# Kernel tuning notes

Hardware: AMD Instinct MI355X
Metric: run time of the kernel (lower is better)

Reference implementation:

```python
import jax, jax.numpy as jnp
import numpy as np

K_NEIGHBORS = 8  # hard-coded k in extract_edge_features
NUM_HEADS = 12


def _sqdist(a, b):
    # a [B,M,3], b [B,N,3] -> squared euclidean distances [B,M,N]
    # (monotone in cdist, so argmax/top-k indices are identical to torch.cdist)
    return jnp.sum((a[:, :, None, :] - b[:, None, :, :]) ** 2, axis=-1)


def _fps(points, num_samples):
    # Farthest point sampling (intended semantics of farthest_point_sampling):
    # iteratively pick the point maximizing the min distance to the selected set.
    B, N, _ = points.shape
    bidx = jnp.arange(B)

    def d_to(idx):  # idx [B] -> squared dist from points[b, idx[b]] to all points [B,N]
        p = points[bidx, idx]  # [B,3]
        return jnp.sum((points - p[:, None, :]) ** 2, axis=-1)

    idx0 = jnp.zeros((B,), jnp.int32)  # deterministic start point

    def step(min_d, _):
        nxt = jnp.argmax(min_d, axis=-1).astype(jnp.int32)  # [B]
        min_d = jnp.minimum(min_d, d_to(nxt))
        return min_d, nxt

    _, rest = jax.lax.scan(step, d_to(idx0), None, length=num_samples - 1)  # rest [M-1,B]
    idxs = jnp.concatenate([idx0[None, :], rest], axis=0).T  # [B,M]
    return jnp.take_along_axis(points, idxs[:, :, None], axis=1)  # [B,M,3]


def _edge_features(points, features, k=K_NEIGHBORS):
    # EdgeAligner.extract_edge_features: kNN by cdist+topk(smallest), then
    # edge = feature - mean(neighbor features)
    d2 = _sqdist(points, points)  # [B,M,M]
    _, nn_idx = jax.lax.top_k(-d2, k)  # [B,M,k] indices of k nearest (incl. self)
    nbr = jax.vmap(lambda f, idx: f[idx])(features, nn_idx)  # [B,M,k,D]
    return features - jnp.mean(nbr, axis=2)


def _mha(x, Wq, bq, Wk, bk, Wv, bv, Wo, bo, num_heads=NUM_HEADS):
    # standard torch nn.MultiheadAttention (self-attention, batch_first)
    B, S, D = x.shape
    dh = D // num_heads
    split = lambda t: t.reshape(B, S, num_heads, dh).transpose(0, 2, 1, 3)
    q = split(x @ Wq + bq)
    k = split(x @ Wk + bk)
    v = split(x @ Wv + bv)
    scale = jnp.asarray(1.0 / np.sqrt(dh), x.dtype)
    att = jax.nn.softmax(jnp.einsum('bhqd,bhkd->bhqk', q, k) * scale, axis=-1)
    o = jnp.einsum('bhqk,bhkd->bhqd', att, v)  # [B,H,S,dh]
    o = o.transpose(0, 2, 1, 3).reshape(B, S, D)
    return o @ Wo + bo


def setup_inputs() -> dict:
    key = jax.random.key(0)
    ks = jax.random.split(key, 8)
    B, N, D = 4, 8192, 768
    s = 0.02
    return {
        'points': jax.random.normal(ks[0], (B, N, 3), jnp.float32),
        'W_embed': jax.random.normal(ks[1], (3, D), jnp.float32) * s,
        'b_embed': jnp.zeros((D,), jnp.float32),
        'Wq': jax.random.normal(ks[2], (D, D), jnp.float32) * s,
        'bq': jnp.zeros((D,), jnp.float32),
        'Wk': jax.random.normal(ks[3], (D, D), jnp.float32) * s,
        'bk': jnp.zeros((D,), jnp.float32),
        'Wv': jax.random.normal(ks[4], (D, D), jnp.float32) * s,
        'bv': jnp.zeros((D,), jnp.float32),
        'Wo': jax.random.normal(ks[5], (D, D), jnp.float32) * s,
        'bo': jnp.zeros((D,), jnp.float32),
        'Ws': jax.random.normal(ks[6], (3, D), jnp.float32) * s,
        'bs': jnp.zeros((D,), jnp.float32),
        'num_samples': 1024,
    }


def reference(points, W_embed, b_embed, Wq, bq, Wk, bk, Wv, bv, Wo, bo, Ws, bs, num_samples):
    # 1) farthest point sampling N -> M
    sampled = _fps(points, num_samples)  # [B,M,3]
    # 2) point embedding (point_embed: Linear(3, 768))
    feats = sampled @ W_embed + b_embed  # [B,M,768]
    # 3) EdgeAligner forward with no external neighbor subsets:
    #    edge features -> self bi-attention -> + spatial embedding
    edge = _edge_features(sampled, feats)  # [B,M,768]
    aligned = _mha(edge, Wq, bq, Wk, bk, Wv, bv, Wo, bo)  # [B,M,768]
    spatial = sampled @ Ws + bs  # spatial_embed: Linear(3, 768)
    return aligned + spatial
```

## Files before the change

kernel.cpp:

```cpp
#include <hip/hip_runtime.h>
#include <float.h>
#include <math.h>

#define BB   4
#define NPTS 8192
#define MS   1024
#define DIM  768
#define NH   12
#define DHD  64
#define KNN  8
#define BMD  (BB*MS*DIM)

typedef float v2f __attribute__((ext_vector_type(2)));

static __device__ __forceinline__ float sqdist3(float ax, float ay, float az,
                                                float bx, float by, float bz) {
  float dx = __fsub_rn(ax, bx);
  float dy = __fsub_rn(ay, by);
  float dz = __fsub_rn(az, bz);
  return __fadd_rn(__fadd_rn(__fmul_rn(dx, dx), __fmul_rn(dy, dy)), __fmul_rn(dz, dz));
}

#define DPP_STAGE(key, ctrl)                                                   \
  {                                                                            \
    unsigned hi_ = (unsigned)((key) >> 32), lo_ = (unsigned)(key);             \
    unsigned nhi_ = (unsigned)__builtin_amdgcn_update_dpp(                     \
        (int)hi_, (int)hi_, (ctrl), 0xf, 0xf, false);                          \
    unsigned nlo_ = (unsigned)__builtin_amdgcn_update_dpp(                     \
        (int)lo_, (int)lo_, (ctrl), 0xf, 0xf, false);                          \
    unsigned long long nk_ = ((unsigned long long)nhi_ << 32) | nlo_;          \
    if (nk_ > (key)) (key) = nk_;                                              \
  }

__global__ __launch_bounds__(512, 1) void fps_kernel(const float* __restrict__ points,
                                                     float* __restrict__ sampled) {
#pragma clang fp contract(off)
  const int b = blockIdx.x;
  const float* pts = points + (size_t)b * NPTS * 3;
  float* smp = sampled + (size_t)b * MS * 3;
  const int tid = threadIdx.x;
  const int lane = tid & 63, w = tid >> 6;

  __shared__ float4 cxyz[NPTS];
  __shared__ unsigned long long red[2][8];

  v2f px[8], py[8], pz[8], md[8];
  const float qx0 = pts[0], qy0 = pts[1], qz0 = pts[2];

  float bv = -INFINITY;
  int bidx = 0;
#pragma unroll
  for (int j = 0; j < 8; ++j) {
    int i0 = 2 * tid + j * 1024;
    float x0 = pts[i0 * 3 + 0], y0 = pts[i0 * 3 + 1], z0 = pts[i0 * 3 + 2];
    float x1 = pts[i0 * 3 + 3], y1 = pts[i0 * 3 + 4], z1 = pts[i0 * 3 + 5];
    px[j] = (v2f){x0, x1}; py[j] = (v2f){y0, y1}; pz[j] = (v2f){z0, z1};
    cxyz[i0]     = make_float4(x0, y0, z0, 0.f);
    cxyz[i0 + 1] = make_float4(x1, y1, z1, 0.f);
    v2f dx = px[j] - qx0, dy = py[j] - qy0, dz = pz[j] - qz0;
    v2f d  = (dx * dx + dy * dy) + dz * dz;
    md[j] = d;
    if (d.x > bv) { bv = d.x; bidx = i0; }
    if (d.y > bv) { bv = d.y; bidx = i0 + 1; }
  }
  if (tid == 0) { smp[0] = qx0; smp[1] = qy0; smp[2] = qz0; }
  __syncthreads();

  for (int s = 1; s < MS; ++s) {
    unsigned long long key =
        ((unsigned long long)__float_as_uint(bv) << 32) |
        (unsigned)(~(unsigned)bidx);

    DPP_STAGE(key, 0xB1);
    DPP_STAGE(key, 0x4E);
    DPP_STAGE(key, 0x141);
    DPP_STAGE(key, 0x140);
    DPP_STAGE(key, 0x142);
    DPP_STAGE(key, 0x143);

    const int buf = s & 1;
    if (lane == 63) red[buf][w] = key;
    __syncthreads();

    unsigned long long kk[8];
#pragma unroll
    for (int i = 0; i < 8; ++i) kk[i] = red[buf][i];
#pragma unroll
    for (int st = 4; st >= 1; st >>= 1)
#pragma unroll
      for (int i = 0; i < 4; ++i)
        if (i < st && kk[i + st] > kk[i]) kk[i] = kk[i + st];

    const unsigned widx = ~(unsigned)(kk[0] & 0xffffffffull);
    const float4 wc = cxyz[widx];
    if (tid == 0) {
      smp[s * 3 + 0] = wc.x; smp[s * 3 + 1] = wc.y; smp[s * 3 + 2] = wc.z;
    }

    bv = -INFINITY; bidx = 0;
#pragma unroll
    for (int j = 0; j < 8; ++j) {
      int i0 = 2 * tid + j * 1024;
      v2f dx = px[j] - wc.x, dy = py[j] - wc.y, dz = pz[j] - wc.z;
      v2f d  = (dx * dx + dy * dy) + dz * dz;
      v2f nm = __builtin_elementwise_min(md[j], d);
      md[j] = nm;
      if (nm.x > bv) { bv = nm.x; bidx = i0; }
      if (nm.y > bv) { bv = nm.y; bidx = i0 + 1; }
    }
  }
}

__global__ void embed_kernel(const float* __restrict__ sampled,
                             const float* __restrict__ W,
                             const float* __restrict__ bias,
                             float* __restrict__ out) {
  int idx = blockIdx.x * blockDim.x + threadIdx.x;
  if (idx >= BMD) return;
  int d = idx % DIM;
  int bm = idx / DIM;
  float x = sampled[bm * 3 + 0], y = sampled[bm * 3 + 1], z = sampled[bm * 3 + 2];
  out[idx] = fmaf(z, W[2 * DIM + d], fmaf(y, W[DIM + d], fmaf(x, W[d], bias[d])));
}

__global__ __launch_bounds__(256) void knn_edge_kernel(const float* __restrict__ sampled,
                                                       const float* __restrict__ feats,
                                                       float* __restrict__ edge) {
  const int bm = blockIdx.x;
  const int b = bm >> 10, m = bm & 1023;
  const float* sp = sampled + (size_t)b * MS * 3;
  const int t = threadIdx.x, lane = t & 63, wid = t >> 6;

  __shared__ float dist[MS];
  __shared__ float redv[4];
  __shared__ int   redi[4];
  __shared__ int   win[KNN];

  const float qx = sp[m * 3 + 0], qy = sp[m * 3 + 1], qz = sp[m * 3 + 2];
#pragma unroll
  for (int j = 0; j < 4; ++j) {
    int i = t + j * 256;
    dist[i] = sqdist3(sp[i * 3 + 0], sp[i * 3 + 1], sp[i * 3 + 2], qx, qy, qz);
  }
  __syncthreads();

  for (int it = 0; it < KNN; ++it) {
    float bv = dist[t]; int bi = t;
#pragma unroll
    for (int j = 1; j < 4; ++j) {
      int i = t + j * 256;
      float v = dist[i];
      if (v < bv || (v == bv && i < bi)) { bv = v; bi = i; }
    }
#pragma unroll
    for (int off = 32; off >= 1; off >>= 1) {
      float ov = __shfl_xor(bv, off);
      int   oi = __shfl_xor(bi, off);
      if (ov < bv || (ov == bv && oi < bi)) { bv = ov; bi = oi; }
    }
    if (lane == 0) { redv[wid] = bv; redi[wid] = bi; }
    __syncthreads();
    if (t == 0) {
      float wv = redv[0]; int wi = redi[0];
#pragma unroll
      for (int w = 1; w < 4; ++w) {
        float ov = redv[w]; int oi = redi[w];
        if (ov < wv || (ov == wv && oi < wi)) { wv = ov; wi = oi; }
      }
      win[it] = wi;
      dist[wi] = FLT_MAX;
    }
    __syncthreads();
  }

  const float* fb = feats + (size_t)b * MS * DIM;
  float* eb = edge + (size_t)b * MS * DIM;
  for (int d = t; d < DIM; d += 256) {
    float acc = 0.f;
#pragma unroll
    for (int i = 0; i < KNN; ++i) acc += fb[(size_t)win[i] * DIM + d];
    eb[(size_t)m * DIM + d] = fb[(size_t)m * DIM + d] - acc * 0.125f;
  }
}

template <int MODE>
__global__ __launch_bounds__(256) void gemm_kernel(const float* __restrict__ A,
                                                   const float* __restrict__ W,
                                                   const float* __restrict__ bias,
                                                   float* __restrict__ C,
                                                   const float* __restrict__ sampled,
                                                   const float* __restrict__ Ws,
                                                   const float* __restrict__ bs) {
  __shared__ float As[16][132];
  __shared__ float Bs[16][68];

  const int t = threadIdx.x;
  const int tx = t & 15, ty = t >> 4;
  const int rowBase = blockIdx.x * 128;
  const int nBase = blockIdx.y * 64;

  float c[8][4] = {};

  const int ar = t >> 1, ac8 = (t & 1) * 8;
  const int br = t >> 4, bc4 = (t & 15) * 4;

  for (int k0 = 0; k0 < DIM; k0 += 16) {
    float4 a0 = *(const float4*)&A[(size_t)(rowBase + ar) * DIM + k0 + ac8];
    float4 a1 = *(const float4*)&A[(size_t)(rowBase + ar) * DIM + k0 + ac8 + 4];
    As[ac8 + 0][ar] = a0.x; As[ac8 + 1][ar] = a0.y;
    As[ac8 + 2][ar] = a0.z; As[ac8 + 3][ar] = a0.w;
    As[ac8 + 4][ar] = a1.x; As[ac8 + 5][ar] = a1.y;
    As[ac8 + 6][ar] = a1.z; As[ac8 + 7][ar] = a1.w;
    float4 wv = *(const float4*)&W[(size_t)(k0 + br) * DIM + nBase + bc4];
    *(float4*)&Bs[br][bc4] = wv;
    __syncthreads();
#pragma unroll
    for (int k = 0; k < 16; ++k) {
      float av[8], bv[4];
      *(float4*)&av[0] = *(const float4*)&As[k][ty * 8];
      *(float4*)&av[4] = *(const float4*)&As[k][ty * 8 + 4];
      *(float4*)bv = *(const float4*)&Bs[k][tx * 4];
#pragma unroll
      for (int i = 0; i < 8; ++i)
#pragma unroll
        for (int j = 0; j < 4; ++j)
          c[i][j] = fmaf(av[i], bv[j], c[i][j]);
    }
    __syncthreads();
  }

#pragma unroll
  for (int i = 0; i < 8; ++i) {
    int row = rowBase + ty * 8 + i;
#pragma unroll
    for (int j = 0; j < 4; ++j) {
      int n = nBase + tx * 4 + j;
      float v = c[i][j] + bias[n];
      if (MODE == 1) {
        const float* sp = sampled + (size_t)row * 3;
        float spt = fmaf(sp[2], Ws[2 * DIM + n], fmaf(sp[1], Ws[DIM + n], fmaf(sp[0], Ws[n], bs[n])));
        v += spt;
      }
      C[(size_t)row * DIM + n] = v;
    }
  }
}

static __device__ __forceinline__ int lidx(int r, int c) {
  return r * 64 + (c ^ ((r & 7) << 2));
}

__global__ __launch_bounds__(256) void attn_kernel(const float* __restrict__ Q,
                                                   const float* __restrict__ K,
                                                   const float* __restrict__ V,
                                                   float* __restrict__ O) {
  const int nrt = MS / 64;
  const int blk = blockIdx.x;
  const int bh = blk / nrt, rt = blk % nrt;
  const int b = bh / NH, h = bh % NH;
  const int t = threadIdx.x, lane = t & 63, w = t >> 6;
  const int rg = lane >> 4, kg = lane & 15;

  __shared__ float Qs[64 * 64];
  __shared__ float Ks[64 * 64];
  __shared__ float Vs[64 * 64];
  __shared__ float Ps[4 * 16 * 64];

  const size_t base = (size_t)(b * MS) * DIM + (size_t)h * DHD;

#pragma unroll
  for (int i = 0; i < 4; ++i) {
    int f = t + i * 256;
    int r = f >> 4, c4 = (f & 15) * 4;
    *(float4*)&Qs[lidx(r, c4)] = *(const float4*)&Q[base + (size_t)(rt * 64 + r) * DIM + c4];
  }

  float m[4], l[4], o[4][4];
#pragma unroll
  for (int i = 0; i < 4; ++i) {
    m[i] = -INFINITY; l[i] = 0.f;
#pragma unroll
    for (int j = 0; j < 4; ++j) o[i][j] = 0.f;
  }

  const int lrow = w * 16 + rg * 4;
  float* Pw = &Ps[w * 16 * 64];

  for (int kt = 0; kt < nrt; ++kt) {
#pragma unroll
    for (int i = 0; i < 4; ++i) {
      int f = t + i * 256;
      int r = f >> 4, c4 = (f & 15) * 4;
      size_t g = base + (size_t)(kt * 64 + r) * DIM + c4;
      *(float4*)&Ks[lidx(r, c4)] = *(const float4*)&K[g];
      *(float4*)&Vs[lidx(r, c4)] = *(const float4*)&V[g];
    }
    __syncthreads();

    float s[4][4] = {};
#pragma unroll 8
    for (int d = 0; d < 64; ++d) {
      float a[4], bb[4];
#pragma unroll
      for (int i = 0; i < 4; ++i) a[i] = Qs[lidx(lrow + i, d)];
#pragma unroll
      for (int j = 0; j < 4; ++j) bb[j] = Ks[lidx(kg + 16 * j, d)];
#pragma unroll
      for (int i = 0; i < 4; ++i)
#pragma unroll
        for (int j = 0; j < 4; ++j) s[i][j] = fmaf(a[i], bb[j], s[i][j]);
    }

#pragma unroll
    for (int i = 0; i < 4; ++i) {
#pragma unroll
      for (int j = 0; j < 4; ++j) s[i][j] *= 0.125f;
      float mt = fmaxf(fmaxf(s[i][0], s[i][1]), fmaxf(s[i][2], s[i][3]));
#pragma unroll
      for (int off = 1; off < 16; off <<= 1) mt = fmaxf(mt, __shfl_xor(mt, off));
      float mn = fmaxf(m[i], mt);
      float corr = expf(m[i] - mn);
      float ps = 0.f;
#pragma unroll
      for (int j = 0; j < 4; ++j) { s[i][j] = expf(s[i][j] - mn); ps += s[i][j]; }
#pragma unroll
      for (int off = 1; off < 16; off <<= 1) ps += __shfl_xor(ps, off);
      l[i] = l[i] * corr + ps;
      m[i] = mn;
#pragma unroll
      for (int j = 0; j < 4; ++j) o[i][j] *= corr;
#pragma unroll
      for (int j = 0; j < 4; ++j) Pw[lidx(rg * 4 + i, kg + 16 * j)] = s[i][j];
    }

#pragma unroll 8
    for (int k = 0; k < 64; ++k) {
      float a[4], bb[4];
#pragma unroll
      for (int i = 0; i < 4; ++i) a[i] = Pw[lidx(rg * 4 + i, k)];
#pragma unroll
      for (int j = 0; j < 4; ++j) bb[j] = Vs[lidx(k, kg + 16 * j)];
#pragma unroll
      for (int i = 0; i < 4; ++i)
#pragma unroll
        for (int j = 0; j < 4; ++j) o[i][j] = fmaf(a[i], bb[j], o[i][j]);
    }
    __syncthreads();
  }

#pragma unroll
  for (int i = 0; i < 4; ++i) {
    int row = rt * 64 + lrow + i;
#pragma unroll
    for (int j = 0; j < 4; ++j)
      O[base + (size_t)row * DIM + kg + 16 * j] = o[i][j] / l[i];
  }
}

extern "C" void kernel_launch(void* const* d_in, const int* in_sizes, int n_in,
                              void* d_out, int out_size, void* d_ws, size_t ws_size,
                              hipStream_t stream) {
  const float* points  = (const float*)d_in[0];
  const float* W_embed = (const float*)d_in[1];
  const float* b_embed = (const float*)d_in[2];
  const float* Wq = (const float*)d_in[3];
  const float* bq = (const float*)d_in[4];
  const float* Wk = (const float*)d_in[5];
  const float* bk = (const float*)d_in[6];
  const float* Wv = (const float*)d_in[7];
  const float* bv = (const float*)d_in[8];
  const float* Wo = (const float*)d_in[9];
  const float* bo = (const float*)d_in[10];
  const float* Ws = (const float*)d_in[11];
  const float* bs = (const float*)d_in[12];

  float* ws = (float*)d_ws;
  float* sampled = ws;
  float* feats   = ws + 16384;
  float* edge    = feats + BMD;
  float* qb      = edge + BMD;
  float* kb      = qb + BMD;
  float* vb      = kb + BMD;
  float* ao      = vb + BMD;

  fps_kernel<<<BB, 512, 0, stream>>>(points, sampled);
  embed_kernel<<<(BMD + 255) / 256, 256, 0, stream>>>(sampled, W_embed, b_embed, feats);
  knn_edge_kernel<<<BB * MS, 256, 0, stream>>>(sampled, feats, edge);

  dim3 ggrid(4096 / 128, DIM / 64);
  gemm_kernel<0><<<ggrid, 256, 0, stream>>>(edge, Wq, bq, qb, nullptr, nullptr, nullptr);
  gemm_kernel<0><<<ggrid, 256, 0, stream>>>(edge, Wk, bk, kb, nullptr, nullptr, nullptr);
  gemm_kernel<0><<<ggrid, 256, 0, stream>>>(edge, Wv, bv, vb, nullptr, nullptr, nullptr);

  attn_kernel<<<BB * NH * (MS / 64), 256, 0, stream>>>(qb, kb, vb, ao);

  gemm_kernel<1><<<ggrid, 256, 0, stream>>>(ao, Wo, bo, (float*)d_out, sampled, Ws, bs);
}
```

Measured before the change: 1.746 ms.

## Widen FPS to 1024 threads with wave-level final reduction and packed math

Doubles the farthest-point-sampling block to 1024 threads so each thread holds 8 points instead of 16. The cross-wave argmax is now done by a single wave with DPP over the 16 partial keys, and the winner is broadcast through shared memory. This costs a second barrier per iteration. Distance math is forced onto v_pk_add/v_pk_mul inline asm. The intent is to shorten the serial per-iteration critical path of the 1023-step loop, trading fewer per-thread ops for extra synchronisation.

```diff
diff --git a/kernel.cpp b/kernel.cpp
--- a/kernel.cpp
+++ b/kernel.cpp
@@ -19,6 +19,22 @@
   float dy = __fsub_rn(ay, by);
   float dz = __fsub_rn(az, bz);
   return __fadd_rn(__fadd_rn(__fmul_rn(dx, dx), __fmul_rn(dy, dy)), __fmul_rn(dz, dz));
+}
+
+static __device__ __forceinline__ v2f pk_sub(v2f a, v2f b) {
+  v2f d;
+  asm("v_pk_add_f32 %0, %1, %2 neg_lo:[0,1] neg_hi:[0,1]" : "=v"(d) : "v"(a), "v"(b));
+  return d;
+}
+static __device__ __forceinline__ v2f pk_mul(v2f a, v2f b) {
+  v2f d;
+  asm("v_pk_mul_f32 %0, %1, %2" : "=v"(d) : "v"(a), "v"(b));
+  return d;
+}
+static __device__ __forceinline__ v2f pk_add(v2f a, v2f b) {
+  v2f d;
+  asm("v_pk_add_f32 %0, %1, %2" : "=v"(d) : "v"(a), "v"(b));
+  return d;
 }
 
 #define DPP_STAGE(key, ctrl)                                                   \
@@ -32,33 +48,36 @@
     if (nk_ > (key)) (key) = nk_;                                              \
   }
 
-__global__ __launch_bounds__(512, 1) void fps_kernel(const float* __restrict__ points,
-                                                     float* __restrict__ sampled) {
+__global__ __launch_bounds__(1024, 1) void fps_kernel(const float* __restrict__ points,
+                                                      float* __restrict__ sampled) {
 #pragma clang fp contract(off)
   const int b = blockIdx.x;
   const float* pts = points + (size_t)b * NPTS * 3;
   float* smp = sampled + (size_t)b * MS * 3;
   const int tid = threadIdx.x;
-  const int lane = tid & 63, w = tid >> 6;
+  const int lane = tid & 63, wid = tid >> 6;
 
   __shared__ float4 cxyz[NPTS];
-  __shared__ unsigned long long red[2][8];
-
-  v2f px[8], py[8], pz[8], md[8];
+  __shared__ unsigned long long red[16];
+  __shared__ float4 fin;
+
+  v2f px[4], py[4], pz[4], md[4];
   const float qx0 = pts[0], qy0 = pts[1], qz0 = pts[2];
 
   float bv = -INFINITY;
   int bidx = 0;
 #pragma unroll
-  for (int j = 0; j < 8; ++j) {
-    int i0 = 2 * tid + j * 1024;
+  for (int j = 0; j < 4; ++j) {
+    int i0 = 2 * tid + j * 2048;
     float x0 = pts[i0 * 3 + 0], y0 = pts[i0 * 3 + 1], z0 = pts[i0 * 3 + 2];
     float x1 = pts[i0 * 3 + 3], y1 = pts[i0 * 3 + 4], z1 = pts[i0 * 3 + 5];
     px[j] = (v2f){x0, x1}; py[j] = (v2f){y0, y1}; pz[j] = (v2f){z0, z1};
     cxyz[i0]     = make_float4(x0, y0, z0, 0.f);
     cxyz[i0 + 1] = make_float4(x1, y1, z1, 0.f);
-    v2f dx = px[j] - qx0, dy = py[j] - qy0, dz = pz[j] - qz0;
-    v2f d  = (dx * dx + dy * dy) + dz * dz;
+    v2f dx = pk_sub(px[j], (v2f){qx0, qx0});
+    v2f dy = pk_sub(py[j], (v2f){qy0, qy0});
+    v2f dz = pk_sub(pz[j], (v2f){qz0, qz0});
+    v2f d  = pk_add(pk_add(pk_mul(dx, dx), pk_mul(dy, dy)), pk_mul(dz, dz));
     md[j] = d;
     if (d.x > bv) { bv = d.x; bidx = i0; }
     if (d.y > bv) { bv = d.y; bidx = i0 + 1; }
@@ -78,31 +97,33 @@
     DPP_STAGE(key, 0x142);
     DPP_STAGE(key, 0x143);
 
-    const int buf = s & 1;
-    if (lane == 63) red[buf][w] = key;
-    __syncthreads();
-
-    unsigned long long kk[8];
-#pragma unroll
-    for (int i = 0; i < 8; ++i) kk[i] = red[buf][i];
-#pragma unroll
-    for (int st = 4; st >= 1; st >>= 1)
-#pragma unroll
-      for (int i = 0; i < 4; ++i)
-        if (i < st && kk[i + st] > kk[i]) kk[i] = kk[i + st];
-
-    const unsigned widx = ~(unsigned)(kk[0] & 0xffffffffull);
-    const float4 wc = cxyz[widx];
-    if (tid == 0) {
-      smp[s * 3 + 0] = wc.x; smp[s * 3 + 1] = wc.y; smp[s * 3 + 2] = wc.z;
-    }
+    if (lane == 63) red[wid] = key;
+    __syncthreads();
+
+    if (wid == 0) {
+      unsigned long long k = red[lane & 15];
+      DPP_STAGE(k, 0xB1);
+      DPP_STAGE(k, 0x4E);
+      DPP_STAGE(k, 0x141);
+      DPP_STAGE(k, 0x140);
+      if (lane == 0) {
+        const unsigned widx = ~(unsigned)(k & 0xffffffffull);
+        float4 wc = cxyz[widx];
+        fin = wc;
+        smp[s * 3 + 0] = wc.x; smp[s * 3 + 1] = wc.y; smp[s * 3 + 2] = wc.z;
+      }
+    }
+    __syncthreads();
+
+    const float4 wc = fin;
+    const v2f wx = (v2f){wc.x, wc.x}, wy = (v2f){wc.y, wc.y}, wz = (v2f){wc.z, wc.z};
 
     bv = -INFINITY; bidx = 0;
 #pragma unroll
-    for (int j = 0; j < 8; ++j) {
-      int i0 = 2 * tid + j * 1024;
-      v2f dx = px[j] - wc.x, dy = py[j] - wc.y, dz = pz[j] - wc.z;
-      v2f d  = (dx * dx + dy * dy) + dz * dz;
+    for (int j = 0; j < 4; ++j) {
+      int i0 = 2 * tid + j * 2048;
+      v2f dx = pk_sub(px[j], wx), dy = pk_sub(py[j], wy), dz = pk_sub(pz[j], wz);
+      v2f d  = pk_add(pk_add(pk_mul(dx, dx), pk_mul(dy, dy)), pk_mul(dz, dz));
       v2f nm = __builtin_elementwise_min(md[j], d);
       md[j] = nm;
       if (nm.x > bv) { bv = nm.x; bidx = i0; }
@@ -383,7 +404,7 @@
   float* vb      = kb + BMD;
   float* ao      = vb + BMD;
 
-  fps_kernel<<<BB, 512, 0, stream>>>(points, sampled);
+  fps_kernel<<<BB, 1024, 0, stream>>>(points, sampled);
   embed_kernel<<<(BMD + 255) / 256, 256, 0, stream>>>(sampled, W_embed, b_embed, feats);
   knn_edge_kernel<<<BB * MS, 256, 0, stream>>>(sampled, feats, edge);
 
```

Measured after the change: 1.938 ms. 1.11x slower.
